# Kernel optimization log

Measured on AMD Instinct MI355X. Metric: run time of the kernel, lower is better.

## Reference

```python
import jax, jax.numpy as jnp
import numpy as np

WINDOW = 15  # window_size from init


def setup_inputs() -> dict:
    key = jax.random.key(0)
    ks = jax.random.split(key, 8)
    B, S, H, G = 16, 4096, 768, 16
    sequence_output = jax.random.normal(ks[0], (B, S, H), dtype=jnp.float32)
    pooled_output = jax.random.normal(ks[1], (B, H), dtype=jnp.float32)
    token_type_ids = jnp.zeros((B, S), dtype=jnp.int64)
    word_mask = jax.random.randint(ks[2], (B, S), 0, 2, dtype=jnp.int64)
    gap_ids = jax.random.randint(ks[3], (B, G), 0, S, dtype=jnp.int64)
    gap_W = 0.02 * jax.random.normal(ks[4], (3 * H,), dtype=jnp.float32)
    gap_b = jnp.zeros((), dtype=jnp.float32)
    cls_W = 0.02 * jax.random.normal(ks[5], (3 * H,), dtype=jnp.float32)
    cls_b = jnp.zeros((), dtype=jnp.float32)
    return {"sequence_output": sequence_output, "pooled_output": pooled_output,
            "token_type_ids": token_type_ids, "word_mask": word_mask,
            "gap_ids": gap_ids, "gap_W": gap_W, "gap_b": gap_b,
            "cls_W": cls_W, "cls_b": cls_b}


def reference(sequence_output, pooled_output, token_type_ids, word_mask,
              gap_ids, gap_W, gap_b, cls_W, cls_b):
    B, S, H = sequence_output.shape
    G = gap_ids.shape[1]
    w = WINDOW
    Wlen = 2 * w + 1

    # gap token embeddings: [B, G, H]
    gaps = jnp.take_along_axis(sequence_output, gap_ids[:, :, None], axis=1)

    base_mask = (token_type_ids == 0) & (word_mask != 0)  # [B, S]

    # Sliding window gather around each gap (equivalent to the original
    # full-sequence masked reduction, since masked entries are exactly 0).
    offsets = jnp.arange(-w, w + 1)  # [Wlen]
    raw_idx = gap_ids[:, :, None] + offsets  # [B, G, Wlen]
    valid = (raw_idx >= 0) & (raw_idx < S)
    idx = jnp.clip(raw_idx, 0, S - 1)
    flat = idx.reshape(B, G * Wlen)
    win_mask = valid & jnp.take_along_axis(base_mask, flat, axis=1).reshape(B, G, Wlen)
    win_vals = jnp.take_along_axis(sequence_output, flat[:, :, None], axis=1).reshape(B, G, Wlen, H)

    # original does max(window * mask): masked positions contribute 0,
    # and the sequence always has positions outside the window -> max with 0
    masked_max = jnp.where(win_mask[..., None], win_vals, -jnp.inf).max(axis=2)
    window_max_pool = jnp.maximum(masked_max, 0.0)  # [B, G, H]
    num_tokens = win_mask.sum(axis=2).astype(jnp.float32)[:, :, None]
    window_avg_pool = jnp.einsum('bgw,bgwh->bgh', win_mask.astype(jnp.float32), win_vals) / num_tokens

    # full-text pooling
    text_masked_max = jnp.where(base_mask[:, :, None], sequence_output, -jnp.inf).max(axis=1)
    text_max_pool = jnp.maximum(text_masked_max, 0.0)  # [B, H]
    text_num = base_mask.sum(axis=1).astype(jnp.float32)[:, None]
    text_avg_pool = jnp.einsum('bs,bsh->bh', base_mask.astype(jnp.float32), sequence_output) / text_num

    gap_features = jnp.concatenate([gaps, window_max_pool, window_avg_pool], axis=-1)  # [B, G, 3H]
    cls_features = jnp.concatenate([pooled_output, text_max_pool, text_avg_pool], axis=-1)  # [B, 3H]

    gap_scores = gap_features @ gap_W + gap_b  # [B, G]
    cls_scores = (cls_features @ cls_W + cls_b)[:, None]  # [B, 1]
    return jnp.concatenate([cls_scores, gap_scores], axis=1)  # [B, 1+G]
```

## Files before the change

kernel.cpp:

```cpp
#include <hip/hip_runtime.h>
#include <math.h>

#define NB 16
#define NS 4096
#define NH 768
#define NG 16
#define WRAD 15
#define WLEN 31
#define NH4 192
#define OUTW (1 + NG)
#define NCH 64
#define CHUNK 64

__device__ inline float4 f4max(float4 a, float4 b) {
    return make_float4(fmaxf(a.x, b.x), fmaxf(a.y, b.y), fmaxf(a.z, b.z), fmaxf(a.w, b.w));
}
__device__ inline float4 f4add(float4 a, float4 b) {
    return make_float4(a.x + b.x, a.y + b.y, a.z + b.z, a.w + b.w);
}
__device__ inline float f4dot(float4 a, float4 b) {
    return a.x * b.x + a.y * b.y + a.z * b.z + a.w * b.w;
}

__device__ inline float block_reduce_192(float v, float* sbuf) {
    int tid = threadIdx.x;
    sbuf[tid] = v;
    if (tid < 64) sbuf[192 + tid] = 0.0f;
    __syncthreads();
    for (int off = 128; off > 0; off >>= 1) {
        if (tid < off) sbuf[tid] += sbuf[tid + off];
        __syncthreads();
    }
    float r = sbuf[0];
    __syncthreads();
    return r;
}

__global__ __launch_bounds__(192) void fused_kernel(
    const float* __restrict__ seq, const int* __restrict__ tt,
    const int* __restrict__ wm, const int* __restrict__ gids,
    const float* __restrict__ gapW, const float* __restrict__ gapb,
    float* __restrict__ pmax, float* __restrict__ psum,
    int* __restrict__ pcnt, float* __restrict__ out) {
    const int blk = blockIdx.x;
    const int tid = threadIdx.x;

    __shared__ float sbuf[256];
    __shared__ int s_idx[CHUNK];
    __shared__ unsigned long long s_wmask;
    __shared__ int s_misc[2];

    const float4 ninf4 = make_float4(-INFINITY, -INFINITY, -INFINITY, -INFINITY);
    const float4 zero4 = make_float4(0.f, 0.f, 0.f, 0.f);

    if (blk < NB * NCH) {
        const int b = blk >> 6;
        const int ss = blk & 63;
        const int s0 = ss * CHUNK;

        if (tid < 64) {
            const int s = s0 + tid;
            const bool v = (tt[b * NS + s] == 0) && (wm[b * NS + s] != 0);
            const unsigned long long m = __ballot(v);
            if (v) {
                const int pos = __popcll(m & ((1ull << tid) - 1ull));
                s_idx[pos] = s;
            }
            if (tid == 0) s_misc[0] = __popcll(m);
        }
        __syncthreads();
        const int n = s_misc[0];

        const float4* rowbase = (const float4*)(seq + (size_t)b * NS * NH);
        float4 mx = ninf4;
        float4 sm = zero4;
        int i = 0;
        for (; i + 8 <= n; i += 8) {
            const int i0 = s_idx[i],     i1 = s_idx[i + 1];
            const int i2 = s_idx[i + 2], i3 = s_idx[i + 3];
            const int i4 = s_idx[i + 4], i5 = s_idx[i + 5];
            const int i6 = s_idx[i + 6], i7 = s_idx[i + 7];
            float4 v0 = rowbase[(size_t)i0 * NH4 + tid];
            float4 v1 = rowbase[(size_t)i1 * NH4 + tid];
            float4 v2 = rowbase[(size_t)i2 * NH4 + tid];
            float4 v3 = rowbase[(size_t)i3 * NH4 + tid];
            float4 v4 = rowbase[(size_t)i4 * NH4 + tid];
            float4 v5 = rowbase[(size_t)i5 * NH4 + tid];
            float4 v6 = rowbase[(size_t)i6 * NH4 + tid];
            float4 v7 = rowbase[(size_t)i7 * NH4 + tid];
            mx = f4max(mx, f4max(f4max(f4max(v0, v1), f4max(v2, v3)),
                                 f4max(f4max(v4, v5), f4max(v6, v7))));
            sm = f4add(sm, f4add(f4add(f4add(v0, v1), f4add(v2, v3)),
                                 f4add(f4add(v4, v5), f4add(v6, v7))));
        }
        if (i + 4 <= n) {
            const int i0 = s_idx[i],     i1 = s_idx[i + 1];
            const int i2 = s_idx[i + 2], i3 = s_idx[i + 3];
            float4 v0 = rowbase[(size_t)i0 * NH4 + tid];
            float4 v1 = rowbase[(size_t)i1 * NH4 + tid];
            float4 v2 = rowbase[(size_t)i2 * NH4 + tid];
            float4 v3 = rowbase[(size_t)i3 * NH4 + tid];
            mx = f4max(mx, f4max(f4max(v0, v1), f4max(v2, v3)));
            sm = f4add(sm, f4add(f4add(v0, v1), f4add(v2, v3)));
            i += 4;
        }
        if (i + 2 <= n) {
            const int i0 = s_idx[i], i1 = s_idx[i + 1];
            float4 v0 = rowbase[(size_t)i0 * NH4 + tid];
            float4 v1 = rowbase[(size_t)i1 * NH4 + tid];
            mx = f4max(mx, f4max(v0, v1));
            sm = f4add(sm, f4add(v0, v1));
            i += 2;
        }
        if (i < n) {
            float4 v = rowbase[(size_t)s_idx[i] * NH4 + tid];
            mx = f4max(mx, v);
            sm = f4add(sm, v);
        }
        const size_t o = ((size_t)(b * NCH + ss)) * NH4 + tid;
        ((float4*)pmax)[o] = mx;
        ((float4*)psum)[o] = sm;
        if (tid == 0) pcnt[b * NCH + ss] = n;
    } else {
        const int bg = blk - NB * NCH;
        const int b = bg >> 4;
        const int g = bg & 15;

        if (tid == 0) s_misc[1] = gids[b * NG + g];
        __syncthreads();
        const int gi = s_misc[1];

        if (tid < 64) {
            bool v = false;
            if (tid < WLEN) {
                const int idx = gi - WRAD + tid;
                v = (idx >= 0) && (idx < NS) && (tt[b * NS + idx] == 0) &&
                    (wm[b * NS + idx] != 0);
            }
            unsigned long long m = __ballot(v);
            if (tid == 0) s_wmask = m;
        }
        __syncthreads();
        const unsigned long long vm = s_wmask;
        const float count = (float)__popcll(vm);

        const float4* rowbase = (const float4*)(seq + (size_t)b * NS * NH);
        const float4 gv = rowbase[(size_t)gi * NH4 + tid];

        float4 mx = ninf4;
        float4 sm = zero4;
#pragma unroll 8
        for (int j = 0; j < WLEN; ++j) {
            int idx = gi - WRAD + j;
            idx = idx < 0 ? 0 : (idx > NS - 1 ? NS - 1 : idx);
            const float4 v = rowbase[(size_t)idx * NH4 + tid];
            const bool val = (vm >> j) & 1ull;
            mx.x = val ? fmaxf(mx.x, v.x) : mx.x;
            mx.y = val ? fmaxf(mx.y, v.y) : mx.y;
            mx.z = val ? fmaxf(mx.z, v.z) : mx.z;
            mx.w = val ? fmaxf(mx.w, v.w) : mx.w;
            sm.x += val ? v.x : 0.f;
            sm.y += val ? v.y : 0.f;
            sm.z += val ? v.z : 0.f;
            sm.w += val ? v.w : 0.f;
        }
        const float4 wmax = f4max(mx, zero4);
        const float4 wavg = make_float4(sm.x / count, sm.y / count,
                                        sm.z / count, sm.w / count);

        const float4* w0 = (const float4*)gapW;
        const float4* w1 = (const float4*)(gapW + NH);
        const float4* w2 = (const float4*)(gapW + 2 * NH);
        float part = f4dot(gv, w0[tid]) + f4dot(wmax, w1[tid]) + f4dot(wavg, w2[tid]);
        float total = block_reduce_192(part, sbuf);
        if (tid == 0) out[b * OUTW + 1 + g] = total + gapb[0];
    }
}

__global__ __launch_bounds__(192) void cls_kernel(
    const float* __restrict__ pooled, const float* __restrict__ pmax,
    const float* __restrict__ psum, const int* __restrict__ pcnt,
    const float* __restrict__ clsW, const float* __restrict__ clsb,
    float* __restrict__ out) {
    const int b = blockIdx.x;
    const int tid = threadIdx.x;
    __shared__ float sbuf[256];

    float c = (tid < NCH) ? (float)pcnt[b * NCH + tid] : 0.f;
    const float count = block_reduce_192(c, sbuf);

    const float4* pm4 = (const float4*)pmax;
    const float4* ps4 = (const float4*)psum;
    float4 mx = make_float4(-INFINITY, -INFINITY, -INFINITY, -INFINITY);
    float4 sm = make_float4(0.f, 0.f, 0.f, 0.f);
#pragma unroll 8
    for (int ch = 0; ch < NCH; ++ch) {
        const size_t o = ((size_t)(b * NCH + ch)) * NH4 + tid;
        mx = f4max(mx, pm4[o]);
        sm = f4add(sm, ps4[o]);
    }
    const float4 zero4 = make_float4(0.f, 0.f, 0.f, 0.f);
    const float4 tmax = f4max(mx, zero4);
    const float4 tavg = make_float4(sm.x / count, sm.y / count,
                                    sm.z / count, sm.w / count);

    const float4* p4 = (const float4*)(pooled + (size_t)b * NH);
    const float4* w0 = (const float4*)clsW;
    const float4* w1 = (const float4*)(clsW + NH);
    const float4* w2 = (const float4*)(clsW + 2 * NH);
    float part = f4dot(p4[tid], w0[tid]) + f4dot(tmax, w1[tid]) + f4dot(tavg, w2[tid]);
    float total = block_reduce_192(part, sbuf);
    if (tid == 0) out[b * OUTW + 0] = total + clsb[0];
}

extern "C" void kernel_launch(void* const* d_in, const int* in_sizes, int n_in,
                              void* d_out, int out_size, void* d_ws, size_t ws_size,
                              hipStream_t stream) {
    const float* seq    = (const float*)d_in[0];
    const float* pooled = (const float*)d_in[1];
    const int*   tt     = (const int*)d_in[2];
    const int*   wm     = (const int*)d_in[3];
    const int*   gids   = (const int*)d_in[4];
    const float* gapW   = (const float*)d_in[5];
    const float* gapb   = (const float*)d_in[6];
    const float* clsW   = (const float*)d_in[7];
    const float* clsb   = (const float*)d_in[8];
    float* out = (float*)d_out;

    float* pmax = (float*)d_ws;
    float* psum = pmax + (size_t)NB * NCH * NH;
    int*   pcnt = (int*)(psum + (size_t)NB * NCH * NH);

    fused_kernel<<<NB * NCH + NB * NG, 192, 0, stream>>>(
        seq, tt, wm, gids, gapW, gapb, pmax, psum, pcnt, out);
    cls_kernel<<<NB, 192, 0, stream>>>(pooled, pmax, psum, pcnt, clsW, clsb, out);
}
```

Before: 299.5 us.

## Fuse cls reduction into main kernel via last-block atomic counter; double chunk size

Removes the separate cls_kernel launch. The last chunk block for each batch, detected with an atomic counter and threadfence, now reduces the partial max, sum and count and writes the cls score. The chunk size also doubles from 64 to 128 rows, which halves the number of partials and needs a two-wavefront ballot compaction. The trade-off is fewer and heavier blocks for the dominant streaming pass, plus a serial tail reduction inside one block per batch.

```diff
diff --git a/kernel.cpp b/kernel.cpp
--- a/kernel.cpp
+++ b/kernel.cpp
@@ -9,8 +9,8 @@
 #define WLEN 31
 #define NH4 192
 #define OUTW (1 + NG)
-#define NCH 64
-#define CHUNK 64
+#define NCH 32
+#define CHUNK 128
 
 __device__ inline float4 f4max(float4 a, float4 b) {
     return make_float4(fmaxf(a.x, b.x), fmaxf(a.y, b.y), fmaxf(a.z, b.z), fmaxf(a.w, b.w));
@@ -36,10 +36,14 @@
     return r;
 }
 
+__device__ int g_cnt[NB];
+
 __global__ __launch_bounds__(192) void fused_kernel(
-    const float* __restrict__ seq, const int* __restrict__ tt,
-    const int* __restrict__ wm, const int* __restrict__ gids,
+    const float* __restrict__ seq, const float* __restrict__ pooled,
+    const int* __restrict__ tt, const int* __restrict__ wm,
+    const int* __restrict__ gids,
     const float* __restrict__ gapW, const float* __restrict__ gapb,
+    const float* __restrict__ clsW, const float* __restrict__ clsb,
     float* __restrict__ pmax, float* __restrict__ psum,
     int* __restrict__ pcnt, float* __restrict__ out) {
     const int blk = blockIdx.x;
@@ -47,27 +51,36 @@
 
     __shared__ float sbuf[256];
     __shared__ int s_idx[CHUNK];
-    __shared__ unsigned long long s_wmask;
+    __shared__ unsigned long long s_wmask[2];
     __shared__ int s_misc[2];
+    __shared__ int s_last;
 
     const float4 ninf4 = make_float4(-INFINITY, -INFINITY, -INFINITY, -INFINITY);
     const float4 zero4 = make_float4(0.f, 0.f, 0.f, 0.f);
 
     if (blk < NB * NCH) {
-        const int b = blk >> 6;
-        const int ss = blk & 63;
+        const int b = blk / NCH;
+        const int ss = blk % NCH;
         const int s0 = ss * CHUNK;
 
-        if (tid < 64) {
+        if (tid < CHUNK) {
             const int s = s0 + tid;
-            const bool v = (tt[b * NS + s] == 0) && (wm[b * NS + s] != 0);
-            const unsigned long long m = __ballot(v);
-            if (v) {
-                const int pos = __popcll(m & ((1ull << tid) - 1ull));
-                s_idx[pos] = s;
+            bool v = (tt[b * NS + s] == 0) && (wm[b * NS + s] != 0);
+            unsigned long long m = __ballot(v);
+            if ((tid & 63) == 0) s_wmask[tid >> 6] = m;
+        }
+        __syncthreads();
+        if (tid < CHUNK) {
+            const int w = tid >> 6, l = tid & 63;
+            const unsigned long long m = s_wmask[w];
+            if ((m >> l) & 1ull) {
+                int pos = (w ? __popcll(s_wmask[0]) : 0) +
+                          __popcll(m & ((1ull << l) - 1ull));
+                s_idx[pos] = s0 + tid;
             }
-            if (tid == 0) s_misc[0] = __popcll(m);
-        }
+        }
+        if (tid == 0)
+            s_misc[0] = __popcll(s_wmask[0]) + __popcll(s_wmask[1]);
         __syncthreads();
         const int n = s_misc[0];
 
@@ -121,6 +134,43 @@
         ((float4*)pmax)[o] = mx;
         ((float4*)psum)[o] = sm;
         if (tid == 0) pcnt[b * NCH + ss] = n;
+
+        __threadfence();
+        if (tid == 0) {
+            const int old = atomicAdd(&g_cnt[b], 1);
+            s_last = (old == NCH - 1);
+            if (s_last) atomicExch(&g_cnt[b], 0);
+        }
+        __syncthreads();
+        if (s_last) {
+            __threadfence();
+
+            float c = (tid < NCH) ? (float)pcnt[b * NCH + tid] : 0.f;
+            const float count = block_reduce_192(c, sbuf);
+
+            const float4* pm4 = (const float4*)pmax;
+            const float4* ps4 = (const float4*)psum;
+            float4 cmx = ninf4;
+            float4 csm = zero4;
+#pragma unroll 8
+            for (int ch = 0; ch < NCH; ++ch) {
+                const size_t oo = ((size_t)(b * NCH + ch)) * NH4 + tid;
+                cmx = f4max(cmx, pm4[oo]);
+                csm = f4add(csm, ps4[oo]);
+            }
+            const float4 tmax = f4max(cmx, zero4);
+            const float4 tavg = make_float4(csm.x / count, csm.y / count,
+                                            csm.z / count, csm.w / count);
+
+            const float4* p4 = (const float4*)(pooled + (size_t)b * NH);
+            const float4* w0 = (const float4*)clsW;
+            const float4* w1 = (const float4*)(clsW + NH);
+            const float4* w2 = (const float4*)(clsW + 2 * NH);
+            float part = f4dot(p4[tid], w0[tid]) + f4dot(tmax, w1[tid]) +
+                         f4dot(tavg, w2[tid]);
+            float total = block_reduce_192(part, sbuf);
+            if (tid == 0) out[b * OUTW + 0] = total + clsb[0];
+        }
     } else {
         const int bg = blk - NB * NCH;
         const int b = bg >> 4;
@@ -138,10 +188,10 @@
                     (wm[b * NS + idx] != 0);
             }
             unsigned long long m = __ballot(v);
-            if (tid == 0) s_wmask = m;
-        }
-        __syncthreads();
-        const unsigned long long vm = s_wmask;
+            if (tid == 0) s_wmask[0] = m;
+        }
+        __syncthreads();
+        const unsigned long long vm = s_wmask[0];
         const float count = (float)__popcll(vm);
 
         const float4* rowbase = (const float4*)(seq + (size_t)b * NS * NH);
@@ -177,42 +227,6 @@
     }
 }
 
-__global__ __launch_bounds__(192) void cls_kernel(
-    const float* __restrict__ pooled, const float* __restrict__ pmax,
-    const float* __restrict__ psum, const int* __restrict__ pcnt,
-    const float* __restrict__ clsW, const float* __restrict__ clsb,
-    float* __restrict__ out) {
-    const int b = blockIdx.x;
-    const int tid = threadIdx.x;
-    __shared__ float sbuf[256];
-
-    float c = (tid < NCH) ? (float)pcnt[b * NCH + tid] : 0.f;
-    const float count = block_reduce_192(c, sbuf);
-
-    const float4* pm4 = (const float4*)pmax;
-    const float4* ps4 = (const float4*)psum;
-    float4 mx = make_float4(-INFINITY, -INFINITY, -INFINITY, -INFINITY);
-    float4 sm = make_float4(0.f, 0.f, 0.f, 0.f);
-#pragma unroll 8
-    for (int ch = 0; ch < NCH; ++ch) {
-        const size_t o = ((size_t)(b * NCH + ch)) * NH4 + tid;
-        mx = f4max(mx, pm4[o]);
-        sm = f4add(sm, ps4[o]);
-    }
-    const float4 zero4 = make_float4(0.f, 0.f, 0.f, 0.f);
-    const float4 tmax = f4max(mx, zero4);
-    const float4 tavg = make_float4(sm.x / count, sm.y / count,
-                                    sm.z / count, sm.w / count);
-
-    const float4* p4 = (const float4*)(pooled + (size_t)b * NH);
-    const float4* w0 = (const float4*)clsW;
-    const float4* w1 = (const float4*)(clsW + NH);
-    const float4* w2 = (const float4*)(clsW + 2 * NH);
-    float part = f4dot(p4[tid], w0[tid]) + f4dot(tmax, w1[tid]) + f4dot(tavg, w2[tid]);
-    float total = block_reduce_192(part, sbuf);
-    if (tid == 0) out[b * OUTW + 0] = total + clsb[0];
-}
-
 extern "C" void kernel_launch(void* const* d_in, const int* in_sizes, int n_in,
                               void* d_out, int out_size, void* d_ws, size_t ws_size,
                               hipStream_t stream) {
@@ -232,6 +246,6 @@
     int*   pcnt = (int*)(psum + (size_t)NB * NCH * NH);
 
     fused_kernel<<<NB * NCH + NB * NG, 192, 0, stream>>>(
-        seq, tt, wm, gids, gapW, gapb, pmax, psum, pcnt, out);
-    cls_kernel<<<NB, 192, 0, stream>>>(pooled, pmax, psum, pcnt, clsW, clsb, out);
-}
+        seq, pooled, tt, wm, gids, gapW, gapb, clsW, clsb,
+        pmax, psum, pcnt, out);
+}
```

After: 358.3 us. 19.6% more time.
